# Kernel optimization log

Hardware: AMD Instinct MI355X
Metric: run time of the kernel (lower is better)

## Reference

```python
import jax, jax.numpy as jnp
import numpy as np
import math

HID = 1024
NH = 16
DH = HID // NH
B, S = 2, 2048

def _rel_shift(x):
    # x: [i, j, b, n] -> Transformer-XL relative shift
    i, j, b, n = x.shape
    xp = jnp.pad(x, ((0, 0), (1, 0), (0, 0), (0, 0)))  # [i, j+1, b, n]
    xp = xp.reshape(j + 1, i, b, n)
    return xp[1:].reshape(i, j, b, n)

def setup_inputs() -> dict:
    key = jax.random.key(0)
    ks = jax.random.split(key, 10)
    sc = 1.0 / math.sqrt(HID)
    return {
        "hidden_states": jax.random.normal(ks[0], (B, S, HID), jnp.float32),
        "r": jax.random.normal(ks[1], (S, HID), jnp.float32),
        "r_w_bias": jax.random.normal(ks[2], (NH, DH), jnp.float32) * 0.02,
        "r_r_bias": jax.random.normal(ks[3], (NH, DH), jnp.float32) * 0.02,
        "Wq": jax.random.normal(ks[4], (HID, HID), jnp.float32) * sc,
        "bq": jnp.zeros((HID,), jnp.float32),
        "Wk": jax.random.normal(ks[5], (HID, HID), jnp.float32) * sc,
        "bk": jnp.zeros((HID,), jnp.float32),
        "Wv": jax.random.normal(ks[6], (HID, HID), jnp.float32) * sc,
        "bv": jnp.zeros((HID,), jnp.float32),
        "Wr": jax.random.normal(ks[7], (HID, HID), jnp.float32) * sc,
    }

def reference(hidden_states, r, r_w_bias, r_r_bias, Wq, bq, Wk, bk, Wv, bv, Wr):
    b, s, h = hidden_states.shape
    # projections (weights stored [in, out])
    q = (hidden_states @ Wq + bq).reshape(b, s, NH, DH).transpose(1, 0, 2, 3)  # [s,b,nh,d]
    k = (hidden_states @ Wk + bk).reshape(b, s, NH, DH).transpose(1, 0, 2, 3)  # [s,b,nh,d]
    v = (hidden_states @ Wv + bv).reshape(b, s, NH, DH).transpose(0, 2, 1, 3)  # [b,nh,s,d]
    r_head_k = (r @ Wr).reshape(s, NH, DH)  # [rlen,nh,d]
    # content (AC) and position (BD) terms
    AC = jnp.einsum('ibnd,jbnd->ijbn', q + r_w_bias, k)
    BD = _rel_shift(jnp.einsum('ibnd,jnd->ijbn', q + r_r_bias, r_head_k))
    scores = (AC + BD).transpose(2, 3, 0, 1) / math.sqrt(DH)  # [b,nh,q,k]
    probs = jax.nn.softmax(scores, axis=-1)
    ctx = jnp.matmul(probs, v)  # [b,nh,q,d]
    ctx = ctx.transpose(0, 2, 1, 3).reshape(b, s, h)
    return ctx
```

## Files before the change

### kernel.cpp

```cpp
#include <hip/hip_runtime.h>
#include <math.h>

#define HID   1024
#define NHEAD 16
#define DHEAD 64
#define BATCH 2
#define SEQ   2048

#define TQ   64
#define TK2  128
#define NW2  191
#define LDP  136
#define LDBT 68

#define KS   1024
#define HEADSZ ((size_t)BATCH * SEQ * HID)

typedef __bf16 bf16_t;
typedef bf16_t bf16x8 __attribute__((ext_vector_type(8)));
typedef bf16_t bf16x4 __attribute__((ext_vector_type(4)));
typedef float  f32x4  __attribute__((ext_vector_type(4)));

__device__ __forceinline__ void load_lds16(const void* g, void* l) {
    __builtin_amdgcn_global_load_lds(
        (const __attribute__((address_space(1))) unsigned int*)g,
        (__attribute__((address_space(3))) unsigned int*)l, 16, 0, 0);
}

__device__ __forceinline__ void wg_barrier() {
    asm volatile("s_waitcnt lgkmcnt(0)" ::: "memory");
    __builtin_amdgcn_s_barrier();
    asm volatile("" ::: "memory");
}

__global__ __launch_bounds__(256) void cast_bf16(
    const float* __restrict__ in, bf16_t* __restrict__ out, int n4)
{
    int g = blockIdx.x * 256 + threadIdx.x;
    if (g >= n4) return;
    float4 v = ((const float4*)in)[g];
    bf16x4 o;
    o[0] = (bf16_t)v.x; o[1] = (bf16_t)v.y;
    o[2] = (bf16_t)v.z; o[3] = (bf16_t)v.w;
    *(bf16x4*)(out + (size_t)g * 4) = o;
}

__global__ __launch_bounds__(256) void transpose_cast3(
    const float* __restrict__ W0, const float* __restrict__ W1,
    const float* __restrict__ W2, bf16_t* __restrict__ WtBase)
{
    __shared__ float t[64][65];
    const int z = blockIdx.z;
    const float* W = (z == 0) ? W0 : (z == 1) ? W1 : W2;
    bf16_t* Wt = WtBase + (size_t)z * 1024 * KS;
    const int tid = threadIdx.x;
    const int n0 = blockIdx.x * 64, k0 = blockIdx.y * 64;
    for (int idx = tid; idx < 1024; idx += 256) {
        int r = idx >> 4, c4 = (idx & 15) * 4;
        float4 v = *(const float4*)(W + (size_t)(k0 + r) * HID + n0 + c4);
        t[r][c4] = v.x; t[r][c4 + 1] = v.y; t[r][c4 + 2] = v.z; t[r][c4 + 3] = v.w;
    }
    __syncthreads();
    for (int idx = tid; idx < 1024; idx += 256) {
        int nr = idx >> 4, c4 = (idx & 15) * 4;
        bf16x4 o;
#pragma unroll
        for (int e = 0; e < 4; e++) o[e] = (bf16_t)t[c4 + e][nr];
        *(bf16x4*)(Wt + (size_t)(n0 + nr) * KS + (k0 + c4)) = o;
    }
}

__global__ __launch_bounds__(256, 3) void gemm_qkv_fused(
    const bf16_t* __restrict__ A, const bf16_t* __restrict__ Wt3,
    const float* __restrict__ bq, const float* __restrict__ bk,
    const float* __restrict__ bv, const float* __restrict__ rrb,
    bf16_t* __restrict__ Cq)
{
    __shared__ bf16_t As[128 * 64];
    __shared__ bf16_t Bs[128 * 64];
    const int tid = threadIdx.x;
    const int w = tid >> 6, lane = tid & 63;
    const int quad = lane >> 4, l16 = lane & 15;
    const int bn = blockIdx.x * 128;
    const int bm = blockIdx.y * 128;
    const int proj = bn >> 10;
    const int vswap = (proj == 2);

    const int srow = tid >> 3;
    const int scg  = (tid & 7) ^ ((tid >> 3) & 7);
    const bf16_t* Ab = A   + (size_t)(bm + srow) * KS + scg * 8;
    const bf16_t* Bb = Wt3 + (size_t)(bn + srow) * KS + scg * 8;

    f32x4 acc[2][8];
#pragma unroll
    for (int i = 0; i < 2; i++)
#pragma unroll
        for (int j = 0; j < 8; j++) {
            acc[i][j][0] = 0.f; acc[i][j][1] = 0.f;
            acc[i][j][2] = 0.f; acc[i][j][3] = 0.f;
        }

    const bf16_t* P1 = vswap ? Bs : As;
    const bf16_t* P2 = vswap ? As : Bs;

    for (int k0 = 0; k0 < KS; k0 += 64) {
#pragma unroll
        for (int j = 0; j < 4; j++) {
            load_lds16(Ab + (size_t)j * 32 * KS + k0, &As[j * 2048 + w * 512]);
            load_lds16(Bb + (size_t)j * 32 * KS + k0, &Bs[j * 2048 + w * 512]);
        }
        __syncthreads();
        bf16x8 af[2][2];
#pragma unroll
        for (int mt = 0; mt < 2; mt++) {
            int r = w * 32 + mt * 16 + l16, rx = r & 7;
            int c0 = (quad ^ rx);
            af[mt][0] = *(const bf16x8*)&P1[r * 64 + c0 * 8];
            af[mt][1] = *(const bf16x8*)&P1[r * 64 + (c0 ^ 4) * 8];
        }
#pragma unroll
        for (int nt = 0; nt < 8; nt++) {
            int r = nt * 16 + l16, rx = r & 7;
            int c0 = (quad ^ rx);
            bf16x8 b0 = *(const bf16x8*)&P2[r * 64 + c0 * 8];
            bf16x8 b1 = *(const bf16x8*)&P2[r * 64 + (c0 ^ 4) * 8];
#pragma unroll
            for (int mt = 0; mt < 2; mt++) {
                acc[mt][nt] = __builtin_amdgcn_mfma_f32_16x16x32_bf16(af[mt][0], b0, acc[mt][nt], 0, 0, 0);
                acc[mt][nt] = __builtin_amdgcn_mfma_f32_16x16x32_bf16(af[mt][1], b1, acc[mt][nt], 0, 0, 0);
            }
        }
        __syncthreads();
    }

#pragma unroll
    for (int mt = 0; mt < 2; mt++)
#pragma unroll
        for (int nt = 0; nt < 8; nt++)
#pragma unroll
            for (int r4 = 0; r4 < 4; r4++) {
                int rowp = w * 32 + mt * 16 + quad * 4 + r4;
                int colp = nt * 16 + l16;
                float v = acc[mt][nt][r4];
                if (!vswap) {
                    int m = bm + rowp, nloc = (bn & 1023) + colp;
                    v += (proj == 0) ? (bq[nloc] + rrb[nloc]) : bk[nloc];
                    int bb = m >> 11, s = m & (SEQ - 1);
                    int nh = nloc >> 6, d = nloc & 63;
                    Cq[(size_t)proj * HEADSZ + (((size_t)(bb * NHEAD + nh) * SEQ + s) * DHEAD) + d] = (bf16_t)v;
                } else {
                    int nloc = (bn & 1023) + rowp, m = bm + colp;
                    v += bv[nloc];
                    int bb = m >> 11, s = m & (SEQ - 1);
                    int nh = nloc >> 6, d = nloc & 63;
                    int j = s & 127;
                    int s2 = (s & ~127) | (((j & 15) << 3) | (j >> 4));
                    Cq[(size_t)2 * HEADSZ + (((size_t)(bb * NHEAD + nh) * DHEAD + d) * SEQ) + s2] = (bf16_t)v;
                }
            }
}

__global__ __launch_bounds__(256, 3) void gemm_r_mfma(
    const bf16_t* __restrict__ A, const bf16_t* __restrict__ Bw,
    bf16_t* __restrict__ C)
{
    __shared__ bf16_t As[128 * 64];
    __shared__ bf16_t Bs[128 * 64];
    const int tid = threadIdx.x;
    const int w = tid >> 6, lane = tid & 63;
    const int quad = lane >> 4, l16 = lane & 15;
    const int bn = blockIdx.x * 128;
    const int bm = blockIdx.y * 128;
    const int srow = tid >> 3;
    const int scg  = (tid & 7) ^ ((tid >> 3) & 7);
    const bf16_t* Ab = A  + (size_t)(bm + srow) * KS + scg * 8;
    const bf16_t* Bb = Bw + (size_t)(bn + srow) * KS + scg * 8;

    f32x4 acc[2][8];
#pragma unroll
    for (int i = 0; i < 2; i++)
#pragma unroll
        for (int j = 0; j < 8; j++) {
            acc[i][j][0] = 0.f; acc[i][j][1] = 0.f;
            acc[i][j][2] = 0.f; acc[i][j][3] = 0.f;
        }

    for (int k0 = 0; k0 < KS; k0 += 64) {
#pragma unroll
        for (int j = 0; j < 4; j++) {
            load_lds16(Ab + (size_t)j * 32 * KS + k0, &As[j * 2048 + w * 512]);
            load_lds16(Bb + (size_t)j * 32 * KS + k0, &Bs[j * 2048 + w * 512]);
        }
        __syncthreads();
        bf16x8 af[2][2];
#pragma unroll
        for (int mt = 0; mt < 2; mt++) {
            int r = w * 32 + mt * 16 + l16, rx = r & 7;
            int c0 = (quad ^ rx);
            af[mt][0] = *(const bf16x8*)&As[r * 64 + c0 * 8];
            af[mt][1] = *(const bf16x8*)&As[r * 64 + (c0 ^ 4) * 8];
        }
#pragma unroll
        for (int nt = 0; nt < 8; nt++) {
            int r = nt * 16 + l16, rx = r & 7;
            int c0 = (quad ^ rx);
            bf16x8 b0 = *(const bf16x8*)&Bs[r * 64 + c0 * 8];
            bf16x8 b1 = *(const bf16x8*)&Bs[r * 64 + (c0 ^ 4) * 8];
#pragma unroll
            for (int mt = 0; mt < 2; mt++) {
                acc[mt][nt] = __builtin_amdgcn_mfma_f32_16x16x32_bf16(af[mt][0], b0, acc[mt][nt], 0, 0, 0);
                acc[mt][nt] = __builtin_amdgcn_mfma_f32_16x16x32_bf16(af[mt][1], b1, acc[mt][nt], 0, 0, 0);
            }
        }
        __syncthreads();
    }
#pragma unroll
    for (int mt = 0; mt < 2; mt++)
#pragma unroll
        for (int nt = 0; nt < 8; nt++)
#pragma unroll
            for (int r4 = 0; r4 < 4; r4++) {
                int rowp = w * 32 + mt * 16 + quad * 4 + r4;
                int colp = nt * 16 + l16;
                int s = bm + rowp, n = bn + colp;
                int nh = n >> 6, d = n & 63;
                C[(((size_t)nh * SEQ + s) * DHEAD) + d] = (bf16_t)acc[mt][nt][r4];
            }
}

__global__ __launch_bounds__(256) void post_qkv_combo(
    const float* __restrict__ r, bf16_t* __restrict__ rS,
    const float* __restrict__ Wr, bf16_t* __restrict__ WtR,
    const bf16_t* __restrict__ Kh, const float* __restrict__ rwb,
    const float* __restrict__ rrb, float* __restrict__ dc,
    bf16_t* __restrict__ zp)
{
    __shared__ float t[64][65];
    const int bid = blockIdx.x;
    const int tid = threadIdx.x;
    if (bid < 2048) {
        int g = bid * 256 + tid;
        float4 v = ((const float4*)r)[g];
        bf16x4 o;
        o[0] = (bf16_t)v.x; o[1] = (bf16_t)v.y;
        o[2] = (bf16_t)v.z; o[3] = (bf16_t)v.w;
        *(bf16x4*)(rS + (size_t)g * 4) = o;
    } else if (bid < 2304) {
        int bb = bid - 2048;
        const int n0 = (bb & 15) * 64, k0 = (bb >> 4) * 64;
        for (int idx = tid; idx < 1024; idx += 256) {
            int rr = idx >> 4, c4 = (idx & 15) * 4;
            float4 v = *(const float4*)(Wr + (size_t)(k0 + rr) * HID + n0 + c4);
            t[rr][c4] = v.x; t[rr][c4 + 1] = v.y; t[rr][c4 + 2] = v.z; t[rr][c4 + 3] = v.w;
        }
        __syncthreads();
        for (int idx = tid; idx < 1024; idx += 256) {
            int nr = idx >> 4, c4 = (idx & 15) * 4;
            bf16x4 o;
#pragma unroll
            for (int e = 0; e < 4; e++) o[e] = (bf16_t)t[c4 + e][nr];
            *(bf16x4*)(WtR + (size_t)(n0 + nr) * KS + (k0 + c4)) = o;
        }
    } else {
        int g = (bid - 2304) * 256 + tid;
        int bn = g >> 11;
        int n = bn & (NHEAD - 1);
        const bf16_t* kr = Kh + (size_t)g * DHEAD;
        float a = 0.f;
#pragma unroll
        for (int c8 = 0; c8 < 8; c8++) {
            bf16x8 kv = *(const bf16x8*)(kr + c8 * 8);
#pragma unroll
            for (int e = 0; e < 8; e++) {
                int d = c8 * 8 + e;
                a = fmaf(rwb[n * DHEAD + d] - rrb[n * DHEAD + d], (float)kv[e], a);
            }
        }
        dc[g] = a;
        if (bid == 2304 && tid < 128) zp[tid] = (bf16_t)0.f;
    }
}

__global__ __launch_bounds__(256, 2) void rel_attn_mfma14(
    const bf16_t* __restrict__ Qh, const bf16_t* __restrict__ Kh,
    const bf16_t* __restrict__ Vth, const bf16_t* __restrict__ Rkh,
    const float* __restrict__ dcorr, const bf16_t* __restrict__ zp,
    float* __restrict__ Out)
{
    __shared__ bf16_t qs[65 * 64];
    __shared__ bf16_t ktP[64 * LDP];
    __shared__ bf16_t vt[64 * 128];
    __shared__ bf16_t rkb[192 * LDBT];
    __shared__ float dco[TK2];

    const int tid = threadIdx.x;
    const int w = tid >> 6, lane = tid & 63;
    const int quad = lane >> 4, l16 = lane & 15;

    const int L = blockIdx.x + (SEQ / TQ) * (blockIdx.y + NHEAD * blockIdx.z);
    const int xcd = L & 7, kk = L >> 3;
    const int nb = xcd * 4 + (kk >> 5);
    const int i0 = (kk & 31) * TQ;
    const int n = nb & (NHEAD - 1), b = nb >> 4;

    const bf16_t* Qb = Qh + ((size_t)(b * NHEAD + n) * SEQ + i0) * DHEAD;
    const bf16_t* Kb = Kh + (size_t)(b * NHEAD + n) * SEQ * DHEAD;
    const bf16_t* Vb = Vth + (size_t)(b * NHEAD + n) * DHEAD * SEQ;
    const bf16_t* Rb = Rkh + (size_t)n * SEQ * DHEAD;
    const float*  Db = dcorr + (size_t)(b * NHEAD + n) * SEQ;

    for (int idx = tid; idx < 65 * 8; idx += 256) {
        int row = idx >> 3, p = idx & 7;
        int g = p ^ (row & 7);
        uint4 val = make_uint4(0, 0, 0, 0);
        if (i0 + row < SEQ) val = *(const uint4*)(Qb + row * DHEAD + g * 8);
        *(uint4*)&qs[row * 64 + p * 8] = val;
    }
    __syncthreads();

    const int rq = 16 * w + l16;
    const int cq0 = quad ^ (rq & 7);
    const bf16x8 aq0 = *(const bf16x8*)&qs[rq * 64 + cq0 * 8];
    const bf16x8 aq1 = *(const bf16x8*)&qs[rq * 64 + (cq0 ^ 4) * 8];

    f32x4 o[4];
    float lsum[4];
#pragma unroll
    for (int t = 0; t < 4; t++) {
        o[t][0] = 0.f; o[t][1] = 0.f; o[t][2] = 0.f; o[t][3] = 0.f;
        lsum[t] = 0.f;
    }
    const float C1 = 0.18033688f;

    const int ltB = (3 - w) * 16;

    for (int j0 = 0; j0 < SEQ; j0 += TK2) {
        const int lstar = 64 + i0 - j0;
        const bool mixed = (lstar > 0) && (lstar < NW2);
        const bool needBd64 = (lstar < 127);

        __syncthreads();
#pragma unroll
        for (int t = 0; t < 4; t++) {
            int r0 = (w + 4 * t) * 8;
            int row = r0 + (lane >> 3);
            int gch = (lane & 7) ^ (row & 7);
            load_lds16(Kb + (size_t)(j0 + row) * DHEAD + gch * 8, &ktP[r0 * 64]);
        }
        const int base1 = SEQ + j0 - i0 - TQ;
#pragma unroll
        for (int t = 0; t < 6; t++) {
            int l0 = (w + 4 * t) * 8;
            int l = l0 + (lane >> 3);
            int rr = base1 + l;
            const bf16_t* rp = (rr < SEQ) ? (Rb + (size_t)rr * DHEAD)
                             : (rr > SEQ) ? (Rb + (size_t)(rr - SEQ - 1) * DHEAD) : zp;
            int gch = (lane & 7) ^ (l & 7);
            load_lds16(rp + gch * 8, &rkb[l0 * 64]);
        }
        if (tid < 32) load_lds16(Db + j0 + tid * 4, dco);
#pragma unroll
        for (int t = 0; t < 4; t++) {
            int d0 = (w + 4 * t) * 4;
            int d = d0 + (lane >> 4);
            int gch = (lane & 15) ^ (d & 15);
            load_lds16(Vb + (size_t)d * SEQ + j0 + gch * 8, &vt[d0 * 128]);
        }
        asm volatile("s_waitcnt vmcnt(4)" ::: "memory");
        __builtin_amdgcn_s_barrier();
        asm volatile("" ::: "memory");

        f32x4 sac[8];
#pragma unroll
        for (int nt = 0; nt < 8; nt++) {
            int r = nt * 16 + l16;
            int c0 = quad ^ (r & 7);
            bf16x8 b0 = *(const bf16x8*)&ktP[r * 64 + c0 * 8];
            bf16x8 b1 = *(const bf16x8*)&ktP[r * 64 + (c0 ^ 4) * 8];
            f32x4 c; c[0] = 0.f; c[1] = 0.f; c[2] = 0.f; c[3] = 0.f;
            c = __builtin_amdgcn_mfma_f32_16x16x32_bf16(aq0, b0, c, 0, 0, 0);
            c = __builtin_amdgcn_mfma_f32_16x16x32_bf16(aq1, b1, c, 0, 0, 0);
            sac[nt] = c;
        }
        f32x4 bdc9[9];
#pragma unroll
        for (int lt8 = 0; lt8 < 9; lt8++) {
            int l = ltB + lt8 * 16 + l16;
            int c0 = quad ^ (l & 7);
            bf16x8 b0 = *(const bf16x8*)&rkb[l * 64 + c0 * 8];
            bf16x8 b1 = *(const bf16x8*)&rkb[l * 64 + (c0 ^ 4) * 8];
            f32x4 c; c[0] = 0.f; c[1] = 0.f; c[2] = 0.f; c[3] = 0.f;
            c = __builtin_amdgcn_mfma_f32_16x16x32_bf16(aq0, b0, c, 0, 0, 0);
            c = __builtin_amdgcn_mfma_f32_16x16x32_bf16(aq1, b1, c, 0, 0, 0);
            bdc9[lt8] = c;
        }
        float bd64 = 0.f;
        if (needBd64 && w >= 2) {
            int l = (w - 2) * 64 + lane;
            int lx = l & 7;
#pragma unroll
            for (int c = 0; c < 8; c++) {
                bf16x8 qv = *(const bf16x8*)&qs[64 * 64 + c * 8];
                bf16x8 rv = *(const bf16x8*)&rkb[l * 64 + (c ^ lx) * 8];
#pragma unroll
                for (int e = 0; e < 8; e++) bd64 = fmaf((float)qv[e], (float)rv[e], bd64);
            }
        }
        wg_barrier();

#pragma unroll
        for (int lt8 = 0; lt8 < 9; lt8++) {
            int l = ltB + lt8 * 16 + l16;
            bf16x4 pk;
#pragma unroll
            for (int r = 0; r < 4; r++) pk[r] = (bf16_t)bdc9[lt8][r];
            *(bf16x4*)&rkb[l * LDBT + 16 * w + quad * 4] = pk;
        }
        if (needBd64 && w >= 2) rkb[((w - 2) * 64 + lane) * LDBT + 64] = (bf16_t)bd64;

        asm volatile("s_waitcnt vmcnt(0)" ::: "memory");
        asm volatile("s_waitcnt lgkmcnt(0)" ::: "memory");
        __builtin_amdgcn_s_barrier();
        asm volatile("" ::: "memory");

        float sv[8][4];
        if (mixed) {
#pragma unroll
            for (int nt = 0; nt < 8; nt++) {
                float dcv = dco[nt * 16 + l16];
#pragma unroll
                for (int r = 0; r < 4; r++) {
                    int il = 16 * w + quad * 4 + r;
                    int jl = nt * 16 + l16;
                    int l = jl + (TQ - 1) - il;
                    int rr = base1 + l;
                    int ip = il + (rr > SEQ ? 1 : 0);
                    float bd = (float)rkb[l * LDBT + ip];
                    sv[nt][r] = sac[nt][r] + dcv + bd;
                }
            }
        } else {
            const int shift = (lstar <= 0) ? 1 : 0;
            const int il0 = 16 * w + quad * 4;
            const int base = (l16 + (TQ - 1) - il0) * LDBT + il0 + shift;
#pragma unroll
            for (int nt = 0; nt < 8; nt++) {
                float dcv = dco[nt * 16 + l16];
#pragma unroll
                for (int r = 0; r < 4; r++) {
                    float bd = (float)rkb[base + nt * 16 * LDBT - r * (LDBT - 1)];
                    sv[nt][r] = sac[nt][r] + dcv + bd;
                }
            }
        }

#pragma unroll
        for (int r = 0; r < 4; r++) {
            float s = 0.f;
#pragma unroll
            for (int nt = 0; nt < 8; nt++) {
                sv[nt][r] = exp2f(sv[nt][r] * C1);
                s += sv[nt][r];
            }
            lsum[r] += s;
        }

#pragma unroll
        for (int r = 0; r < 4; r++) {
            bf16x8 px;
#pragma unroll
            for (int nt = 0; nt < 8; nt++) px[nt] = (bf16_t)sv[nt][r];
            *(bf16x8*)&ktP[(16 * w + quad * 4 + r) * LDP + l16 * 8] = px;
        }

        bf16x8 pa[4];
#pragma unroll
        for (int c = 0; c < 4; c++)
            pa[c] = *(const bf16x8*)&ktP[(16 * w + l16) * LDP + c * 32 + quad * 8];
#pragma unroll
        for (int nt = 0; nt < 4; nt++) {
#pragma unroll
            for (int c = 0; c < 4; c++) {
                int dv = nt * 16 + l16;
                int gch = (4 * c + quad) ^ (dv & 15);
                bf16x8 vb = *(const bf16x8*)&vt[dv * 128 + gch * 8];
                o[nt] = __builtin_amdgcn_mfma_f32_16x16x32_bf16(pa[c], vb, o[nt], 0, 0, 0);
            }
        }
    }

    float inv[4];
#pragma unroll
    for (int r = 0; r < 4; r++) {
        float s = lsum[r];
        s += __shfl_xor(s, 1); s += __shfl_xor(s, 2);
        s += __shfl_xor(s, 4); s += __shfl_xor(s, 8);
        inv[r] = 1.f / s;
    }
#pragma unroll
    for (int nt = 0; nt < 4; nt++)
#pragma unroll
        for (int r = 0; r < 4; r++) {
            int gi = i0 + 16 * w + quad * 4 + r;
            Out[(size_t)(b * SEQ + gi) * HID + n * DHEAD + nt * 16 + l16] = o[nt][r] * inv[r];
        }
}

extern "C" void kernel_launch(void* const* d_in, const int* in_sizes, int n_in,
                              void* d_out, int out_size, void* d_ws, size_t ws_size,
                              hipStream_t stream) {
    const float* hs  = (const float*)d_in[0];
    const float* r   = (const float*)d_in[1];
    const float* rwb = (const float*)d_in[2];
    const float* rrb = (const float*)d_in[3];
    const float* Wq  = (const float*)d_in[4];
    const float* bq  = (const float*)d_in[5];
    const float* Wk  = (const float*)d_in[6];
    const float* bk  = (const float*)d_in[7];
    const float* Wv  = (const float*)d_in[8];
    const float* bv  = (const float*)d_in[9];
    const float* Wr  = (const float*)d_in[10];

    bf16_t* ws0 = (bf16_t*)d_ws;
    bf16_t* hsS = ws0;
    bf16_t* Wt3 = ws0 + (size_t)4096 * KS;
    bf16_t* Qh  = Wt3 + (size_t)3072 * KS;
    bf16_t* Kh  = Qh + HEADSZ;
    bf16_t* Vh  = Kh + HEADSZ;
    bf16_t* Rh  = Vh + HEADSZ;
    bf16_t* rS  = ws0;
    bf16_t* WtR = ws0 + (size_t)2048 * KS;
    float*  dcG = (float*)(ws0 + (size_t)3072 * KS);
    bf16_t* zp  = ws0 + (size_t)3072 * KS + 2 * BATCH * NHEAD * SEQ;

    dim3 blk(256);

    cast_bf16<<<4096, blk, 0, stream>>>(hs, hsS, (BATCH * SEQ * HID) / 4);
    transpose_cast3<<<dim3(16, 16, 3), blk, 0, stream>>>(Wq, Wk, Wv, Wt3);
    gemm_qkv_fused<<<dim3(24, 32), blk, 0, stream>>>(hsS, Wt3, bq, bk, bv, rrb, Qh);

    post_qkv_combo<<<2560, blk, 0, stream>>>(r, rS, Wr, WtR, Kh, rwb, rrb, dcG, zp);

    gemm_r_mfma<<<dim3(8, 16), blk, 0, stream>>>(rS, WtR, Rh);

    rel_attn_mfma14<<<dim3(SEQ / TQ, NHEAD, BATCH), blk, 0, stream>>>(
        Qh, Kh, Vh, Rh, dcG, zp, (float*)d_out);
}
```

Before: 301.9 us.

## Merge prep kernels and fuse R projection and key correction into QKV GEMM

All input casts and weight transposes (hidden states, Wq/Wk/Wv, r, Wr) now run in one prep kernel. The R projection GEMM is folded into the QKV GEMM launch as extra column blocks, and the per-key bias-correction dot product is computed in the K-projection epilogue with lane shuffles instead of a separate pass that re-read K. This cuts the launch count from six to three and removes the reload of K, at the cost of idle early-exit blocks in the padded grid and more work in the epilogue. The workspace layout is reorganised so the buffers no longer alias.

```diff
diff --git a/kernel.cpp b/kernel.cpp
--- a/kernel.cpp
+++ b/kernel.cpp
@@ -33,63 +33,96 @@
     asm volatile("" ::: "memory");
 }
 
-__global__ __launch_bounds__(256) void cast_bf16(
-    const float* __restrict__ in, bf16_t* __restrict__ out, int n4)
-{
-    int g = blockIdx.x * 256 + threadIdx.x;
-    if (g >= n4) return;
-    float4 v = ((const float4*)in)[g];
-    bf16x4 o;
-    o[0] = (bf16_t)v.x; o[1] = (bf16_t)v.y;
-    o[2] = (bf16_t)v.z; o[3] = (bf16_t)v.w;
-    *(bf16x4*)(out + (size_t)g * 4) = o;
-}
-
-__global__ __launch_bounds__(256) void transpose_cast3(
+__global__ __launch_bounds__(256) void prep_combo(
+    const float* __restrict__ hs, bf16_t* __restrict__ hsS,
     const float* __restrict__ W0, const float* __restrict__ W1,
-    const float* __restrict__ W2, bf16_t* __restrict__ WtBase)
+    const float* __restrict__ W2, bf16_t* __restrict__ Wt3,
+    const float* __restrict__ r, bf16_t* __restrict__ rS,
+    const float* __restrict__ Wr, bf16_t* __restrict__ WtR,
+    bf16_t* __restrict__ zp)
 {
     __shared__ float t[64][65];
-    const int z = blockIdx.z;
-    const float* W = (z == 0) ? W0 : (z == 1) ? W1 : W2;
-    bf16_t* Wt = WtBase + (size_t)z * 1024 * KS;
+    const int bid = blockIdx.x;
     const int tid = threadIdx.x;
-    const int n0 = blockIdx.x * 64, k0 = blockIdx.y * 64;
-    for (int idx = tid; idx < 1024; idx += 256) {
-        int r = idx >> 4, c4 = (idx & 15) * 4;
-        float4 v = *(const float4*)(W + (size_t)(k0 + r) * HID + n0 + c4);
-        t[r][c4] = v.x; t[r][c4 + 1] = v.y; t[r][c4 + 2] = v.z; t[r][c4 + 3] = v.w;
-    }
-    __syncthreads();
-    for (int idx = tid; idx < 1024; idx += 256) {
-        int nr = idx >> 4, c4 = (idx & 15) * 4;
+    if (bid < 4096) {
+        int g = bid * 256 + tid;
+        float4 v = ((const float4*)hs)[g];
         bf16x4 o;
-#pragma unroll
-        for (int e = 0; e < 4; e++) o[e] = (bf16_t)t[c4 + e][nr];
-        *(bf16x4*)(Wt + (size_t)(n0 + nr) * KS + (k0 + c4)) = o;
+        o[0] = (bf16_t)v.x; o[1] = (bf16_t)v.y;
+        o[2] = (bf16_t)v.z; o[3] = (bf16_t)v.w;
+        *(bf16x4*)(hsS + (size_t)g * 4) = o;
+        if (bid == 0 && tid < 128) zp[tid] = (bf16_t)0.f;
+    } else if (bid < 4864) {
+        int bb = bid - 4096;
+        int z = bb >> 8, tt = bb & 255;
+        const float* W = (z == 0) ? W0 : (z == 1) ? W1 : W2;
+        bf16_t* Wt = Wt3 + (size_t)z * 1024 * KS;
+        const int n0 = (tt & 15) * 64, k0 = (tt >> 4) * 64;
+        for (int idx = tid; idx < 1024; idx += 256) {
+            int rr = idx >> 4, c4 = (idx & 15) * 4;
+            float4 v = *(const float4*)(W + (size_t)(k0 + rr) * HID + n0 + c4);
+            t[rr][c4] = v.x; t[rr][c4 + 1] = v.y; t[rr][c4 + 2] = v.z; t[rr][c4 + 3] = v.w;
+        }
+        __syncthreads();
+        for (int idx = tid; idx < 1024; idx += 256) {
+            int nr = idx >> 4, c4 = (idx & 15) * 4;
+            bf16x4 o;
+#pragma unroll
+            for (int e = 0; e < 4; e++) o[e] = (bf16_t)t[c4 + e][nr];
+            *(bf16x4*)(Wt + (size_t)(n0 + nr) * KS + (k0 + c4)) = o;
+        }
+    } else if (bid < 6912) {
+        int g = (bid - 4864) * 256 + tid;
+        float4 v = ((const float4*)r)[g];
+        bf16x4 o;
+        o[0] = (bf16_t)v.x; o[1] = (bf16_t)v.y;
+        o[2] = (bf16_t)v.z; o[3] = (bf16_t)v.w;
+        *(bf16x4*)(rS + (size_t)g * 4) = o;
+    } else {
+        int tt = bid - 6912;
+        const int n0 = (tt & 15) * 64, k0 = (tt >> 4) * 64;
+        for (int idx = tid; idx < 1024; idx += 256) {
+            int rr = idx >> 4, c4 = (idx & 15) * 4;
+            float4 v = *(const float4*)(Wr + (size_t)(k0 + rr) * HID + n0 + c4);
+            t[rr][c4] = v.x; t[rr][c4 + 1] = v.y; t[rr][c4 + 2] = v.z; t[rr][c4 + 3] = v.w;
+        }
+        __syncthreads();
+        for (int idx = tid; idx < 1024; idx += 256) {
+            int nr = idx >> 4, c4 = (idx & 15) * 4;
+            bf16x4 o;
+#pragma unroll
+            for (int e = 0; e < 4; e++) o[e] = (bf16_t)t[c4 + e][nr];
+            *(bf16x4*)(WtR + (size_t)(n0 + nr) * KS + (k0 + c4)) = o;
+        }
     }
 }
 
-__global__ __launch_bounds__(256, 3) void gemm_qkv_fused(
+__global__ __launch_bounds__(256, 3) void gemm_qkv_r(
     const bf16_t* __restrict__ A, const bf16_t* __restrict__ Wt3,
+    const bf16_t* __restrict__ rS, const bf16_t* __restrict__ WtR,
     const float* __restrict__ bq, const float* __restrict__ bk,
     const float* __restrict__ bv, const float* __restrict__ rrb,
-    bf16_t* __restrict__ Cq)
+    const float* __restrict__ rwb,
+    bf16_t* __restrict__ Cq, bf16_t* __restrict__ Rh,
+    float* __restrict__ dc)
 {
+    const int x = blockIdx.x, y = blockIdx.y;
+    const bool isR = (x >= 24);
+    if (isR && y >= 16) return;
     __shared__ bf16_t As[128 * 64];
     __shared__ bf16_t Bs[128 * 64];
     const int tid = threadIdx.x;
     const int w = tid >> 6, lane = tid & 63;
     const int quad = lane >> 4, l16 = lane & 15;
-    const int bn = blockIdx.x * 128;
-    const int bm = blockIdx.y * 128;
-    const int proj = bn >> 10;
+    const int bn = (isR ? (x - 24) : x) * 128;
+    const int bm = y * 128;
+    const int proj = isR ? 3 : (bn >> 10);
     const int vswap = (proj == 2);
 
     const int srow = tid >> 3;
     const int scg  = (tid & 7) ^ ((tid >> 3) & 7);
-    const bf16_t* Ab = A   + (size_t)(bm + srow) * KS + scg * 8;
-    const bf16_t* Bb = Wt3 + (size_t)(bn + srow) * KS + scg * 8;
+    const bf16_t* Ab = (isR ? rS : A)    + (size_t)(bm + srow) * KS + scg * 8;
+    const bf16_t* Bb = (isR ? WtR : Wt3) + (size_t)(bn + srow) * KS + scg * 8;
 
     f32x4 acc[2][8];
 #pragma unroll
@@ -131,6 +164,22 @@
             }
         }
         __syncthreads();
+    }
+
+    if (proj == 3) {
+#pragma unroll
+        for (int mt = 0; mt < 2; mt++)
+#pragma unroll
+            for (int nt = 0; nt < 8; nt++)
+#pragma unroll
+                for (int r4 = 0; r4 < 4; r4++) {
+                    int rowp = w * 32 + mt * 16 + quad * 4 + r4;
+                    int colp = nt * 16 + l16;
+                    int s = bm + rowp, nn = bn + colp;
+                    int nh = nn >> 6, d = nn & 63;
+                    Rh[(((size_t)nh * SEQ + s) * DHEAD) + d] = (bf16_t)acc[mt][nt][r4];
+                }
+        return;
     }
 
 #pragma unroll
@@ -158,126 +207,38 @@
                     Cq[(size_t)2 * HEADSZ + (((size_t)(bb * NHEAD + nh) * DHEAD + d) * SEQ) + s2] = (bf16_t)v;
                 }
             }
-}
-
-__global__ __launch_bounds__(256, 3) void gemm_r_mfma(
-    const bf16_t* __restrict__ A, const bf16_t* __restrict__ Bw,
-    bf16_t* __restrict__ C)
-{
-    __shared__ bf16_t As[128 * 64];
-    __shared__ bf16_t Bs[128 * 64];
-    const int tid = threadIdx.x;
-    const int w = tid >> 6, lane = tid & 63;
-    const int quad = lane >> 4, l16 = lane & 15;
-    const int bn = blockIdx.x * 128;
-    const int bm = blockIdx.y * 128;
-    const int srow = tid >> 3;
-    const int scg  = (tid & 7) ^ ((tid >> 3) & 7);
-    const bf16_t* Ab = A  + (size_t)(bm + srow) * KS + scg * 8;
-    const bf16_t* Bb = Bw + (size_t)(bn + srow) * KS + scg * 8;
-
-    f32x4 acc[2][8];
-#pragma unroll
-    for (int i = 0; i < 2; i++)
-#pragma unroll
-        for (int j = 0; j < 8; j++) {
-            acc[i][j][0] = 0.f; acc[i][j][1] = 0.f;
-            acc[i][j][2] = 0.f; acc[i][j][3] = 0.f;
-        }
-
-    for (int k0 = 0; k0 < KS; k0 += 64) {
-#pragma unroll
-        for (int j = 0; j < 4; j++) {
-            load_lds16(Ab + (size_t)j * 32 * KS + k0, &As[j * 2048 + w * 512]);
-            load_lds16(Bb + (size_t)j * 32 * KS + k0, &Bs[j * 2048 + w * 512]);
-        }
-        __syncthreads();
-        bf16x8 af[2][2];
-#pragma unroll
-        for (int mt = 0; mt < 2; mt++) {
-            int r = w * 32 + mt * 16 + l16, rx = r & 7;
-            int c0 = (quad ^ rx);
-            af[mt][0] = *(const bf16x8*)&As[r * 64 + c0 * 8];
-            af[mt][1] = *(const bf16x8*)&As[r * 64 + (c0 ^ 4) * 8];
-        }
+
+    if (proj == 1) {
+        const int hb = (bn & 1023) >> 6;
+        float wd[8], bkv[8];
 #pragma unroll
         for (int nt = 0; nt < 8; nt++) {
-            int r = nt * 16 + l16, rx = r & 7;
-            int c0 = (quad ^ rx);
-            bf16x8 b0 = *(const bf16x8*)&Bs[r * 64 + c0 * 8];
-            bf16x8 b1 = *(const bf16x8*)&Bs[r * 64 + (c0 ^ 4) * 8];
-#pragma unroll
-            for (int mt = 0; mt < 2; mt++) {
-                acc[mt][nt] = __builtin_amdgcn_mfma_f32_16x16x32_bf16(af[mt][0], b0, acc[mt][nt], 0, 0, 0);
-                acc[mt][nt] = __builtin_amdgcn_mfma_f32_16x16x32_bf16(af[mt][1], b1, acc[mt][nt], 0, 0, 0);
-            }
-        }
-        __syncthreads();
-    }
-#pragma unroll
-    for (int mt = 0; mt < 2; mt++)
-#pragma unroll
-        for (int nt = 0; nt < 8; nt++)
-#pragma unroll
-            for (int r4 = 0; r4 < 4; r4++) {
-                int rowp = w * 32 + mt * 16 + quad * 4 + r4;
-                int colp = nt * 16 + l16;
-                int s = bm + rowp, n = bn + colp;
-                int nh = n >> 6, d = n & 63;
-                C[(((size_t)nh * SEQ + s) * DHEAD) + d] = (bf16_t)acc[mt][nt][r4];
-            }
-}
-
-__global__ __launch_bounds__(256) void post_qkv_combo(
-    const float* __restrict__ r, bf16_t* __restrict__ rS,
-    const float* __restrict__ Wr, bf16_t* __restrict__ WtR,
-    const bf16_t* __restrict__ Kh, const float* __restrict__ rwb,
-    const float* __restrict__ rrb, float* __restrict__ dc,
-    bf16_t* __restrict__ zp)
-{
-    __shared__ float t[64][65];
-    const int bid = blockIdx.x;
-    const int tid = threadIdx.x;
-    if (bid < 2048) {
-        int g = bid * 256 + tid;
-        float4 v = ((const float4*)r)[g];
-        bf16x4 o;
-        o[0] = (bf16_t)v.x; o[1] = (bf16_t)v.y;
-        o[2] = (bf16_t)v.z; o[3] = (bf16_t)v.w;
-        *(bf16x4*)(rS + (size_t)g * 4) = o;
-    } else if (bid < 2304) {
-        int bb = bid - 2048;
-        const int n0 = (bb & 15) * 64, k0 = (bb >> 4) * 64;
-        for (int idx = tid; idx < 1024; idx += 256) {
-            int rr = idx >> 4, c4 = (idx & 15) * 4;
-            float4 v = *(const float4*)(Wr + (size_t)(k0 + rr) * HID + n0 + c4);
-            t[rr][c4] = v.x; t[rr][c4 + 1] = v.y; t[rr][c4 + 2] = v.z; t[rr][c4 + 3] = v.w;
-        }
-        __syncthreads();
-        for (int idx = tid; idx < 1024; idx += 256) {
-            int nr = idx >> 4, c4 = (idx & 15) * 4;
-            bf16x4 o;
-#pragma unroll
-            for (int e = 0; e < 4; e++) o[e] = (bf16_t)t[c4 + e][nr];
-            *(bf16x4*)(WtR + (size_t)(n0 + nr) * KS + (k0 + c4)) = o;
-        }
-    } else {
-        int g = (bid - 2304) * 256 + tid;
-        int bn = g >> 11;
-        int n = bn & (NHEAD - 1);
-        const bf16_t* kr = Kh + (size_t)g * DHEAD;
-        float a = 0.f;
-#pragma unroll
-        for (int c8 = 0; c8 < 8; c8++) {
-            bf16x8 kv = *(const bf16x8*)(kr + c8 * 8);
-#pragma unroll
-            for (int e = 0; e < 8; e++) {
-                int d = c8 * 8 + e;
-                a = fmaf(rwb[n * DHEAD + d] - rrb[n * DHEAD + d], (float)kv[e], a);
-            }
-        }
-        dc[g] = a;
-        if (bid == 2304 && tid < 128) zp[tid] = (bf16_t)0.f;
+            int nloc = (bn & 1023) + nt * 16 + l16;
+            wd[nt] = rwb[nloc] - rrb[nloc];
+            bkv[nt] = bk[nloc];
+        }
+#pragma unroll
+        for (int mt = 0; mt < 2; mt++)
+#pragma unroll
+            for (int r4 = 0; r4 < 4; r4++)
+#pragma unroll
+                for (int h = 0; h < 2; h++) {
+                    float sdc = 0.f;
+#pragma unroll
+                    for (int nt4 = 0; nt4 < 4; nt4++) {
+                        int nt = h * 4 + nt4;
+                        float vb = acc[mt][nt][r4] + bkv[nt];
+                        sdc = fmaf(wd[nt], (float)(bf16_t)vb, sdc);
+                    }
+                    sdc += __shfl_xor(sdc, 1); sdc += __shfl_xor(sdc, 2);
+                    sdc += __shfl_xor(sdc, 4); sdc += __shfl_xor(sdc, 8);
+                    if (l16 == 0) {
+                        int m = bm + w * 32 + mt * 16 + quad * 4 + r4;
+                        int bb = m >> 11, s = m & (SEQ - 1);
+                        int nh = hb + h;
+                        dc[(size_t)(bb * NHEAD + nh) * SEQ + s] = sdc;
+                    }
+                }
     }
 }
 
@@ -521,27 +482,25 @@
     const float* bv  = (const float*)d_in[9];
     const float* Wr  = (const float*)d_in[10];
 
+    const size_t M1 = (size_t)1024 * 1024;
     bf16_t* ws0 = (bf16_t*)d_ws;
     bf16_t* hsS = ws0;
-    bf16_t* Wt3 = ws0 + (size_t)4096 * KS;
-    bf16_t* Qh  = Wt3 + (size_t)3072 * KS;
-    bf16_t* Kh  = Qh + HEADSZ;
-    bf16_t* Vh  = Kh + HEADSZ;
-    bf16_t* Rh  = Vh + HEADSZ;
-    bf16_t* rS  = ws0;
-    bf16_t* WtR = ws0 + (size_t)2048 * KS;
-    float*  dcG = (float*)(ws0 + (size_t)3072 * KS);
-    bf16_t* zp  = ws0 + (size_t)3072 * KS + 2 * BATCH * NHEAD * SEQ;
+    bf16_t* Wt3 = ws0 + 4 * M1;
+    bf16_t* Qh  = ws0 + 7 * M1;
+    bf16_t* Kh  = ws0 + 11 * M1;
+    bf16_t* Vh  = ws0 + 15 * M1;
+    bf16_t* Rh  = ws0 + 19 * M1;
+    bf16_t* rS  = ws0 + 21 * M1;
+    bf16_t* WtR = ws0 + 23 * M1;
+    float*  dcG = (float*)(ws0 + 24 * M1);
+    bf16_t* zp  = ws0 + 24 * M1 + 2 * BATCH * NHEAD * SEQ;
 
     dim3 blk(256);
 
-    cast_bf16<<<4096, blk, 0, stream>>>(hs, hsS, (BATCH * SEQ * HID) / 4);
-    transpose_cast3<<<dim3(16, 16, 3), blk, 0, stream>>>(Wq, Wk, Wv, Wt3);
-    gemm_qkv_fused<<<dim3(24, 32), blk, 0, stream>>>(hsS, Wt3, bq, bk, bv, rrb, Qh);
-
-    post_qkv_combo<<<2560, blk, 0, stream>>>(r, rS, Wr, WtR, Kh, rwb, rrb, dcG, zp);
-
-    gemm_r_mfma<<<dim3(8, 16), blk, 0, stream>>>(rS, WtR, Rh);
+    prep_combo<<<7168, blk, 0, stream>>>(hs, hsS, Wq, Wk, Wv, Wt3, r, rS, Wr, WtR, zp);
+
+    gemm_qkv_r<<<dim3(32, 32), blk, 0, stream>>>(
+        hsS, Wt3, rS, WtR, bq, bk, bv, rrb, rwb, Qh, Rh, dcG);
 
     rel_attn_mfma14<<<dim3(SEQ / TQ, NHEAD, BATCH), blk, 0, stream>>>(
         Qh, Kh, Vh, Rh, dcG, zp, (float*)d_out);
```

Result: faster. 289.7 us (-4.0%).
